# Kernel optimization log

Measured on AMD Instinct MI355X. Metric: run time of the kernel, lower is better.

The kernel has to match this reference:

```python
import jax, jax.numpy as jnp
import numpy as np

N = 100000      # nodes
E = 1600000     # edges
NF, EF = 8, 4   # raw node/edge feature dims
HID = 64        # hidden_dim
HEADS = 4
C = HID // HEADS  # per-head channels = 16
L = 3           # num_layers
NEG_SLOPE = 0.2 # PyG GATConv leaky_relu slope
LN_EPS = 1e-5


def setup_inputs():
    key = jax.random.key(0)
    ks = jax.random.split(key, 16)
    s = 0.1
    return {
        "x": jax.random.normal(ks[0], (N, NF), dtype=jnp.float32),
        "edge_index": jax.random.randint(ks[1], (2, E), 0, N, dtype=jnp.int32),
        "edge_attr": jax.random.normal(ks[2], (E, EF), dtype=jnp.float32),
        "node_w": jax.random.normal(ks[3], (NF, HID), dtype=jnp.float32) * s,
        "node_b": jnp.zeros((HID,), jnp.float32),
        "edge_w": jax.random.normal(ks[4], (EF, HID), dtype=jnp.float32) * s,
        "edge_b": jnp.zeros((HID,), jnp.float32),
        "lin_w": jax.random.normal(ks[5], (L, HID, HEADS * C), dtype=jnp.float32) * s,
        "lin_edge_w": jax.random.normal(ks[6], (L, HID, HEADS * C), dtype=jnp.float32) * s,
        "att_src": jax.random.normal(ks[7], (L, HEADS, C), dtype=jnp.float32) * s,
        "att_dst": jax.random.normal(ks[8], (L, HEADS, C), dtype=jnp.float32) * s,
        "att_edge": jax.random.normal(ks[9], (L, HEADS, C), dtype=jnp.float32) * s,
        "gat_bias": jnp.zeros((L, HID), jnp.float32),
        "ln_gamma": jnp.ones((L, HID), jnp.float32),
        "ln_beta": jnp.zeros((L, HID), jnp.float32),
    }


def _layer_norm(x, g, b):
    mu = jnp.mean(x, axis=-1, keepdims=True)
    var = jnp.mean(jnp.square(x - mu), axis=-1, keepdims=True)
    return (x - mu) * jax.lax.rsqrt(var + LN_EPS) * g + b


def _gat_conv(x, src, dst, e_proj, lin_w, lin_edge_w, a_src_w, a_dst_w, a_edge_w, bias):
    """PyG GATConv (concat=True, edge_dim, self-loops with fill='mean').
    x: [N,HID]; src/dst: [E'] (already include self loops); e_proj: [E',HID]."""
    n = x.shape[0]
    xs = (x @ lin_w).reshape(n, HEADS, C)                    # [N,H,C]
    ea = (e_proj @ lin_edge_w).reshape(-1, HEADS, C)         # [E',H,C]
    a_src = jnp.einsum('nhc,hc->nh', xs, a_src_w)            # [N,H]
    a_dst = jnp.einsum('nhc,hc->nh', xs, a_dst_w)            # [N,H]
    a_edge = jnp.einsum('ehc,hc->eh', ea, a_edge_w)          # [E',H]
    alpha = a_src[src] + a_dst[dst] + a_edge                 # [E',H]
    alpha = jax.nn.leaky_relu(alpha, NEG_SLOPE)
    # segment softmax over edges sharing a destination node
    amax = jax.ops.segment_max(alpha, dst, num_segments=n)   # [N,H]
    ex = jnp.exp(alpha - amax[dst])
    denom = jax.ops.segment_sum(ex, dst, num_segments=n)     # [N,H]
    w = ex / (denom[dst] + 1e-16)                            # [E',H]
    msg = xs[src] * w[:, :, None]                            # [E',H,C]
    out = jax.ops.segment_sum(msg, dst, num_segments=n)      # [N,H,C]
    return out.reshape(n, HEADS * C) + bias


def reference(x, edge_index, edge_attr, node_w, node_b, edge_w, edge_b,
              lin_w, lin_edge_w, att_src, att_dst, att_edge, gat_bias,
              ln_gamma, ln_beta):
    h = x @ node_w + node_b                                  # [N,HID]
    e = edge_attr @ edge_w + edge_b                          # [E,HID]
    src, dst = edge_index[0], edge_index[1]
    # add self loops once (same for all layers); edge_attr fill = per-dst mean
    ones = jnp.ones((E,), h.dtype)
    deg = jax.ops.segment_sum(ones, dst, num_segments=N)     # [N]
    e_mean = jax.ops.segment_sum(e, dst, num_segments=N) / jnp.maximum(deg, 1.0)[:, None]
    loop = jnp.arange(N, dtype=src.dtype)
    src_f = jnp.concatenate([src, loop])
    dst_f = jnp.concatenate([dst, loop])
    e_f = jnp.concatenate([e, e_mean], axis=0)               # [E+N,HID]
    for i in range(L):
        residual = h
        h = _gat_conv(h, src_f, dst_f, e_f, lin_w[i], lin_edge_w[i],
                      att_src[i], att_dst[i], att_edge[i], gat_bias[i])
        h = _layer_norm(h + residual, ln_gamma[i], ln_beta[i])
        h = jax.nn.relu(h)
    return h
```

## Files before the change

### kernel.cpp

```cpp
#include <hip/hip_runtime.h>


#define LRELU_SLOPE 0.2f
#define LOG2E 1.4426950408889634f
#define P1B 512
#define NBKT_MAX 512

typedef float f32x2 __attribute__((ext_vector_type(2)));

#ifdef __has_builtin
#if __has_builtin(__builtin_amdgcn_fdot2_f32_bf16)
#define HAS_BF16DOT 1
#endif
#endif
#ifndef HAS_BF16DOT
#define HAS_BF16DOT 0
#endif

#if HAS_BF16DOT
typedef __bf16 bf16x2_t __attribute__((ext_vector_type(2)));
#endif

__device__ __forceinline__ f32x2 fp8lo(unsigned int v) {
    return __builtin_amdgcn_cvt_pk_f32_fp8((int)v, false);
}
__device__ __forceinline__ f32x2 fp8hi(unsigned int v) {
    return __builtin_amdgcn_cvt_pk_f32_fp8((int)v, true);
}
__device__ __forceinline__ ushort f2bf(float x) {
    unsigned int b = __float_as_uint(x);
    return (ushort)((b + 0x7fffu + ((b >> 16) & 1u)) >> 16);
}
__device__ __forceinline__ unsigned int pack2bf(float a, float b) {
    return (unsigned int)f2bf(a) | ((unsigned int)f2bf(b) << 16);
}
__device__ __forceinline__ float bf_lo(unsigned int v) { return __uint_as_float(v << 16); }
__device__ __forceinline__ float bf_hi(unsigned int v) { return __uint_as_float(v & 0xffff0000u); }

__device__ __forceinline__ float dot2bf(unsigned int a, unsigned int b, float c) {
#if HAS_BF16DOT
    return __builtin_amdgcn_fdot2_f32_bf16(__builtin_bit_cast(bf16x2_t, a),
                                           __builtin_bit_cast(bf16x2_t, b), c, false);
#else
    return fmaf(bf_lo(a), bf_lo(b), fmaf(bf_hi(a), bf_hi(b), c));
#endif
}

__global__ void k_prep0(const float* __restrict__ lin_edge_w,
                        const float* __restrict__ att_edge,
                        const float* __restrict__ edge_w,
                        const float* __restrict__ edge_b,
                        float* __restrict__ Mc,
                        const float* __restrict__ x, const float* __restrict__ nw,
                        const float* __restrict__ nb, ushort* __restrict__ hbf,
                        int n_nodes)
{
    __shared__ float we[3][64][4];
    int t = threadIdx.x;
    if (blockIdx.x == 0) {
        if (t < 192) {
            int l = t >> 6, k = t & 63;
            for (int h = 0; h < 4; ++h) {
                float acc = 0.f;
                #pragma unroll
                for (int c = 0; c < 16; ++c)
                    acc = fmaf(lin_edge_w[l*4096 + k*64 + h*16 + c],
                               att_edge[l*64 + h*16 + c], acc);
                we[l][k][h] = acc;
            }
        }
        __syncthreads();
        if (t < 48) {
            int l = t >> 4, k4 = (t >> 2) & 3, h = t & 3;
            float acc = 0.f;
            for (int k = 0; k < 64; ++k)
                acc = fmaf(edge_w[k4*64 + k], we[l][k][h], acc);
            Mc[l*16 + k4*4 + h] = acc * LOG2E;
        }
        if (t >= 64 && t < 76) {
            int u = t - 64, l = u >> 2, h = u & 3;
            float acc = 0.f;
            for (int k = 0; k < 64; ++k)
                acc = fmaf(edge_b[k], we[l][k][h], acc);
            Mc[48 + l*4 + h] = acc * LOG2E;
        }
        return;
    }
    int idx = (blockIdx.x - 1) * blockDim.x + t;
    int n = idx >> 6, j = idx & 63;
    if (n >= n_nodes) return;
    float acc = nb[j];
    #pragma unroll
    for (int k = 0; k < 8; ++k) acc = fmaf(x[n*8 + k], nw[k*64 + j], acc);
    hbf[(size_t)n*64 + j] = f2bf(acc);
}

__global__ __launch_bounds__(256) void k_hist1(const int* __restrict__ dst,
                                               int* __restrict__ C,
                                               int E, int chunk, int nbkt) {
    __shared__ int h[NBKT_MAX];
    int b = blockIdx.x, t = threadIdx.x;
    for (int i = t; i < nbkt; i += 256) h[i] = 0;
    __syncthreads();
    int e0 = b*chunk, e1 = min(e0 + chunk, E);
    for (int e = e0 + t; e < e1; e += 256)
        atomicAdd(&h[dst[e] >> 8], 1);
    __syncthreads();
    for (int i = t; i < nbkt; i += 256) C[i*P1B + b] = h[i];
}

__global__ void k_scanA(const int* __restrict__ in, int* __restrict__ out,
                        int* __restrict__ bsum, int n) {
    __shared__ int s[1024];
    int i = blockIdx.x*1024 + threadIdx.x;
    s[threadIdx.x] = (i < n) ? in[i] : 0;
    __syncthreads();
    for (int off = 1; off < 1024; off <<= 1) {
        int t = (threadIdx.x >= off) ? s[threadIdx.x - off] : 0;
        __syncthreads();
        s[threadIdx.x] += t;
        __syncthreads();
    }
    if (i < n) out[i] = s[threadIdx.x];
    if (threadIdx.x == 1023) bsum[blockIdx.x] = s[1023];
}

__global__ void k_scanB(int* bsum, int nb) {
    __shared__ int s[1024];
    int t = threadIdx.x;
    int own = (t < nb) ? bsum[t] : 0;
    s[t] = own;
    __syncthreads();
    for (int off = 1; off < 1024; off <<= 1) {
        int v = (t >= off) ? s[t - off] : 0;
        __syncthreads();
        s[t] += v;
        __syncthreads();
    }
    if (t < nb) bsum[t] = s[t] - own;
}

__device__ __forceinline__ int scanned(const int* S, const int* bsum, int idx) {
    return S[idx] + bsum[idx >> 10];
}

__global__ __launch_bounds__(256) void k_scat1(const int* __restrict__ dst,
        const int* __restrict__ srcv, const float4* __restrict__ ea,
        const int* __restrict__ S, const int* __restrict__ bsum,
        uint2* __restrict__ brec, int E, int chunk, int nbkt) {
    __shared__ int base[NBKT_MAX];
    __shared__ int cur[NBKT_MAX];
    int b = blockIdx.x, t = threadIdx.x;
    for (int i = t; i < nbkt; i += 256) {
        int flat = i*P1B + b;
        base[i] = flat ? scanned(S, bsum, flat - 1) : 0;
        cur[i] = 0;
    }
    __syncthreads();
    int e0 = b*chunk, e1 = min(e0 + chunk, E);
    for (int e = e0 + t; e < e1; e += 256) {
        int d = dst[e];
        int bin = d >> 8;
        int lr = atomicAdd(&cur[bin], 1);
        int slot = base[bin] + lr;
        float4 v = ea[e];
        unsigned int p = (unsigned int)__builtin_amdgcn_cvt_pk_fp8_f32(v.x, v.y, 0, false);
        p = (unsigned int)__builtin_amdgcn_cvt_pk_fp8_f32(v.z, v.w, (int)p, true);
        uint2 r;
        r.x = (unsigned int)srcv[e] | ((unsigned int)(d & 255) << 24);
        r.y = p;
        brec[slot] = r;
    }
}

__global__ __launch_bounds__(256) void k_csr(const uint2* __restrict__ brec,
        const int* __restrict__ S, const int* __restrict__ bsum,
        uint2* __restrict__ recs, int* __restrict__ rowptr, int* __restrict__ perm,
        float4* __restrict__ ea_mean, int nbkt, int NN, int E) {
    int bkt = blockIdx.x, t = threadIdx.x;
    __shared__ int cnt[256], exc[256], cur[256], ssc[256], dk[256];
    int ib = bkt*P1B - 1, ie = (bkt + 1)*P1B - 1;
    int seg_b = bkt ? scanned(S, bsum, ib) : 0;
    int seg_e = scanned(S, bsum, ie);
    cnt[t] = 0; cur[t] = 0;
    __syncthreads();
    for (int i = seg_b + t; i < seg_e; i += 256)
        atomicAdd(&cnt[brec[i].x >> 24], 1);
    __syncthreads();
    ssc[t] = cnt[t];
    __syncthreads();
    for (int off = 1; off < 256; off <<= 1) {
        int v = (t >= off) ? ssc[t - off] : 0;
        __syncthreads();
        ssc[t] += v;
        __syncthreads();
    }
    exc[t] = ssc[t] - cnt[t];
    __syncthreads();
    int g = bkt*256 + t;
    bool valid = (g < NN);
    int row_b = seg_b + exc[t];
    if (valid) rowptr[g] = row_b;
    if (bkt == nbkt - 1 && t == 0) rowptr[NN] = E;
    int myd = valid ? cnt[t] : 0x7FFFFFFF;
    dk[t] = myd;
    __syncthreads();
    int w0 = t & ~15;
    int rank = 0;
    #pragma unroll
    for (int j = 0; j < 16; ++j) {
        int od = dk[w0 + j];
        rank += (int)((od < myd) || (od == myd && (w0 + j) < t));
    }
    perm[bkt*256 + w0 + rank] = g;
    for (int i = seg_b + t; i < seg_e; i += 256) {
        uint2 r = brec[i];
        int dl = (int)(r.x >> 24);
        int slot = seg_b + exc[dl] + atomicAdd(&cur[dl], 1);
        r.x &= 0x00FFFFFFu;
        recs[slot] = r;
    }
    __syncthreads();
    if (valid) {
        int deg = cnt[t];
        float sx = 0.f, sy = 0.f, sz = 0.f, sw = 0.f;
        for (int i = 0; i < deg; ++i) {
            unsigned int p = recs[row_b + i].y;
            f32x2 lo = fp8lo(p), hi = fp8hi(p);
            sx += lo.x; sy += lo.y; sz += hi.x; sw += hi.y;
        }
        float inv = deg ? 1.f / (float)deg : 0.f;
        ea_mean[g] = make_float4(sx*inv, sy*inv, sz*inv, sw*inv);
    }
    if (bkt == nbkt - 1 && t < 8 && E > 0) recs[E + t] = recs[E - 1];
}

__global__ __launch_bounds__(256) void k_proj(const ushort* __restrict__ hbf,
        const float* __restrict__ lw,
        const float* __restrict__ asw,
        const float* __restrict__ adw,
        ushort* __restrict__ xs2, float* __restrict__ a_src4,
        float* __restrict__ a_dst4, int n_nodes)
{
    __shared__ unsigned int Wp[2048];
    for (int i = threadIdx.x; i < 2048; i += 256) {
        int k2 = i >> 6, c = i & 63;
        Wp[i] = pack2bf(lw[(k2*2)*64 + c], lw[(k2*2+1)*64 + c]);
    }
    __syncthreads();
    int lane = threadIdx.x & 63, wid = threadIdx.x >> 6;
    float as_w = asw[lane] * LOG2E, ad_w = adw[lane] * LOG2E;
    int nquads = (n_nodes + 3) >> 2;
    int nlast = n_nodes - 1;
    for (int q = blockIdx.x*4 + wid; q < nquads; q += gridDim.x*4) {
        int n0 = q << 2;
        int n1 = min(n0+1, nlast), n2 = min(n0+2, nlast), n3 = min(n0+3, nlast);
        const uint4* r0p = (const uint4*)(hbf + (size_t)n0*64);
        const uint4* r1p = (const uint4*)(hbf + (size_t)n1*64);
        const uint4* r2p = (const uint4*)(hbf + (size_t)n2*64);
        const uint4* r3p = (const uint4*)(hbf + (size_t)n3*64);
        float acc0 = 0.f, acc1 = 0.f, acc2 = 0.f, acc3 = 0.f;
        #pragma unroll
        for (int qq = 0; qq < 8; ++qq) {
            uint4 u0 = r0p[qq], u1 = r1p[qq], u2 = r2p[qq], u3 = r3p[qq];
            unsigned int w0 = Wp[(qq*4+0)*64 + lane];
            unsigned int w1 = Wp[(qq*4+1)*64 + lane];
            unsigned int w2 = Wp[(qq*4+2)*64 + lane];
            unsigned int w3 = Wp[(qq*4+3)*64 + lane];
            acc0 = dot2bf(u0.w, w3, dot2bf(u0.z, w2, dot2bf(u0.y, w1, dot2bf(u0.x, w0, acc0))));
            acc1 = dot2bf(u1.w, w3, dot2bf(u1.z, w2, dot2bf(u1.y, w1, dot2bf(u1.x, w0, acc1))));
            acc2 = dot2bf(u2.w, w3, dot2bf(u2.z, w2, dot2bf(u2.y, w1, dot2bf(u2.x, w0, acc2))));
            acc3 = dot2bf(u3.w, w3, dot2bf(u3.z, w2, dot2bf(u3.y, w1, dot2bf(u3.x, w0, acc3))));
        }
        xs2[(size_t)n0*64 + lane] = f2bf(acc0);
        xs2[(size_t)n1*64 + lane] = f2bf(acc1);
        xs2[(size_t)n2*64 + lane] = f2bf(acc2);
        xs2[(size_t)n3*64 + lane] = f2bf(acc3);
        #define ARED(ACC, NJ) { \
            float ps = (ACC)*as_w, pd = (ACC)*ad_w; \
            ps += __shfl_xor(ps,1,16); pd += __shfl_xor(pd,1,16); \
            ps += __shfl_xor(ps,2,16); pd += __shfl_xor(pd,2,16); \
            ps += __shfl_xor(ps,4,16); pd += __shfl_xor(pd,4,16); \
            ps += __shfl_xor(ps,8,16); pd += __shfl_xor(pd,8,16); \
            if ((lane & 15) == 0) { \
                a_src4[(NJ)*4 + (lane>>4)] = ps; \
                a_dst4[(NJ)*4 + (lane>>4)] = pd; \
            } }
        ARED(acc0, n0) ARED(acc1, n1) ARED(acc2, n2) ARED(acc3, n3)
        #undef ARED
    }
}

__global__ __launch_bounds__(256) void k_gat(const uint4* __restrict__ xs4,
        const float* __restrict__ a_src4, const float* __restrict__ a_dst4,
        const int* __restrict__ rowptr, const uint2* __restrict__ recs,
        const float4* __restrict__ ea_mean, const int* __restrict__ perm,
        const float* __restrict__ Mc,
        const float* __restrict__ c0,
        const float* __restrict__ bias, const float* __restrict__ lng,
        const float* __restrict__ lnb,
        const ushort* __restrict__ hbf_in, ushort* __restrict__ hbf_out,
        float* __restrict__ out_f32, int last, int n_nodes)
{
    int lane = threadIdx.x & 63;
    int q4 = lane >> 4;
    int gq = blockIdx.x*16 + (threadIdx.x >> 6)*4 + q4;
    bool active = (gq < n_nodes);
    int n = active ? perm[gq] : 0;
    int l4  = lane & 15;
    int k8  = l4 & 7;
    int hB  = k8 >> 1;
    int grp = l4 >> 3;
    int cb = k8 * 8;
    uint4 rr = *(const uint4*)(hbf_in + (size_t)n*64 + cb);
    float4 eam = ea_mean[n];
    float m0 = Mc[hB], m1 = Mc[4+hB], m2 = Mc[8+hB], m3 = Mc[12+hB];
    float c0v = c0[hB];
    float adv = a_dst4[n*4 + hB];
    float cc = c0v + adv;
    int rb = rowptr[n], re = active ? rowptr[n + 1] : rb;

    float denL = 0.f;
    float a0=0.f,a1=0.f,a2=0.f,a3=0.f,a4=0.f,a5=0.f,a6=0.f,a7=0.f;

    if (rb < re) {
        int bmax = re - grp;
        uint2 rc = recs[rb + grp];
        uint2 rn = recs[rb + 2 + grp];
        float asc = a_src4[(int)rc.x*4 + hB];
        uint4 xc = xs4[(unsigned)rc.x*8u + (unsigned)k8];
        #pragma unroll 2
        for (int b = rb; b < re; b += 2) {
            uint2 r2 = recs[b + 4 + grp];
            float asn = a_src4[(int)rn.x*4 + hB];
            uint4 xn = xs4[(unsigned)rn.x*8u + (unsigned)k8];
            f32x2 e01 = fp8lo(rc.y), e23 = fp8hi(rc.y);
            float al = fmaf(e01.x, m0, fmaf(e01.y, m1,
                       fmaf(e23.x, m2, fmaf(e23.y, m3, cc)))) + asc;
            al = fmaxf(al, LRELU_SLOPE * al);
            float ev = (b < bmax) ? exp2f(al) : 0.f;
            denL += ev;
            a0 = fmaf(bf_lo(xc.x), ev, a0); a1 = fmaf(bf_hi(xc.x), ev, a1);
            a2 = fmaf(bf_lo(xc.y), ev, a2); a3 = fmaf(bf_hi(xc.y), ev, a3);
            a4 = fmaf(bf_lo(xc.z), ev, a4); a5 = fmaf(bf_hi(xc.z), ev, a5);
            a6 = fmaf(bf_lo(xc.w), ev, a6); a7 = fmaf(bf_hi(xc.w), ev, a7);
            rc = rn; rn = r2; asc = asn; xc = xn;
        }
    }
    denL += __shfl_xor(denL, 8);
    a0 += __shfl_xor(a0, 8); a1 += __shfl_xor(a1, 8);
    a2 += __shfl_xor(a2, 8); a3 += __shfl_xor(a3, 8);
    a4 += __shfl_xor(a4, 8); a5 += __shfl_xor(a5, 8);
    a6 += __shfl_xor(a6, 8); a7 += __shfl_xor(a7, 8);
    float ael = (re > rb)
        ? fmaf(eam.x, m0, fmaf(eam.y, m1, fmaf(eam.z, m2, fmaf(eam.w, m3, c0v))))
        : 0.f;
    float alS = a_src4[n*4 + hB] + adv + ael;
    alS = fmaxf(alS, LRELU_SLOPE * alS);
    float evS = exp2f(alS);
    float denF = denL + evS;
    uint4 vs = xs4[(unsigned)n*8u + (unsigned)k8];
    a0 = fmaf(bf_lo(vs.x), evS, a0); a1 = fmaf(bf_hi(vs.x), evS, a1);
    a2 = fmaf(bf_lo(vs.y), evS, a2); a3 = fmaf(bf_hi(vs.y), evS, a3);
    a4 = fmaf(bf_lo(vs.z), evS, a4); a5 = fmaf(bf_hi(vs.z), evS, a5);
    a6 = fmaf(bf_lo(vs.w), evS, a6); a7 = fmaf(bf_hi(vs.w), evS, a7);
    float inv = 1.f / (denF + 1e-16f);
    const float4* bp = (const float4*)(bias + cb);
    float4 b0 = bp[0], b1 = bp[1];
    float o0 = a0*inv + b0.x + bf_lo(rr.x), o1 = a1*inv + b0.y + bf_hi(rr.x);
    float o2 = a2*inv + b0.z + bf_lo(rr.y), o3 = a3*inv + b0.w + bf_hi(rr.y);
    float o4 = a4*inv + b1.x + bf_lo(rr.z), o5 = a5*inv + b1.y + bf_hi(rr.z);
    float o6 = a6*inv + b1.z + bf_lo(rr.w), o7 = a7*inv + b1.w + bf_hi(rr.w);
    float s1 = o0+o1+o2+o3+o4+o5+o6+o7;
    s1 += __shfl_xor(s1, 1); s1 += __shfl_xor(s1, 2); s1 += __shfl_xor(s1, 4);
    float mu = s1 * 0.015625f;
    float d0=o0-mu,d1=o1-mu,d2=o2-mu,d3=o3-mu,d4=o4-mu,d5=o5-mu,d6=o6-mu,d7=o7-mu;
    float s2 = d0*d0+d1*d1+d2*d2+d3*d3+d4*d4+d5*d5+d6*d6+d7*d7;
    s2 += __shfl_xor(s2, 1); s2 += __shfl_xor(s2, 2); s2 += __shfl_xor(s2, 4);
    float rs = rsqrtf(s2 * 0.015625f + 1e-5f);
    const float4* gp = (const float4*)(lng + cb);
    const float4* zp = (const float4*)(lnb + cb);
    float4 g0 = gp[0], g1 = gp[1], z0 = zp[0], z1 = zp[1];
    float y0 = fmaxf(d0*rs*g0.x + z0.x, 0.f), y1 = fmaxf(d1*rs*g0.y + z0.y, 0.f);
    float y2 = fmaxf(d2*rs*g0.z + z0.z, 0.f), y3 = fmaxf(d3*rs*g0.w + z0.w, 0.f);
    float y4 = fmaxf(d4*rs*g1.x + z1.x, 0.f), y5 = fmaxf(d5*rs*g1.y + z1.y, 0.f);
    float y6 = fmaxf(d6*rs*g1.z + z1.z, 0.f), y7 = fmaxf(d7*rs*g1.w + z1.w, 0.f);
    if (grp == 0 && active) {
        if (last) {
            float4* outp = (float4*)(out_f32 + (size_t)n*64 + cb);
            outp[0] = make_float4(y0, y1, y2, y3);
            outp[1] = make_float4(y4, y5, y6, y7);
        } else {
            uint4 pk;
            pk.x = pack2bf(y0, y1); pk.y = pack2bf(y2, y3);
            pk.z = pack2bf(y4, y5); pk.w = pack2bf(y6, y7);
            *(uint4*)(hbf_out + (size_t)n*64 + cb) = pk;
        }
    }
}

extern "C" void kernel_launch(void* const* d_in, const int* in_sizes, int n_in,
                              void* d_out, int out_size, void* d_ws, size_t ws_size,
                              hipStream_t stream) {
    const float* x          = (const float*)d_in[0];
    const int*   ei         = (const int*)d_in[1];
    const float* edge_attr  = (const float*)d_in[2];
    const float* node_w     = (const float*)d_in[3];
    const float* node_b     = (const float*)d_in[4];
    const float* edge_w     = (const float*)d_in[5];
    const float* edge_b     = (const float*)d_in[6];
    const float* lin_w      = (const float*)d_in[7];
    const float* lin_edge_w = (const float*)d_in[8];
    const float* att_src    = (const float*)d_in[9];
    const float* att_dst    = (const float*)d_in[10];
    const float* att_edge   = (const float*)d_in[11];
    const float* gat_bias   = (const float*)d_in[12];
    const float* ln_g       = (const float*)d_in[13];
    const float* ln_b       = (const float*)d_in[14];

    int NN = in_sizes[0] / 8;
    int E  = in_sizes[1] / 2;
    const int* src = ei;
    const int* dst = ei + E;

    int nbkt = (NN + 255) >> 8;
    int ntot = nbkt * P1B;
    int chunk = (E + P1B - 1) / P1B;

    char* wsp = (char*)d_ws;
    size_t off = 0;
    auto alloc = [&](size_t bytes) -> void* {
        off = (off + 255) & ~(size_t)255;
        void* p = wsp + off;
        off += bytes;
        return p;
    };
    ushort* h_bf    = (ushort*)alloc((size_t)NN * 64 * 2);
    ushort* xs2     = (ushort*)alloc((size_t)NN * 64 * 2);
    float*  a_src4  = (float*)alloc((size_t)NN * 4 * 4);
    float*  a_dst4  = (float*)alloc((size_t)NN * 4 * 4);
    uint2*  recs    = (uint2*)alloc((size_t)(E + 8) * 8);
    uint2*  brec    = (uint2*)alloc((size_t)E * 8);
    float4* ea_mean = (float4*)alloc((size_t)NN * 16);
    int*    rowptr  = (int*)alloc((size_t)(NN + 1) * 4);
    int*    perm    = (int*)alloc((size_t)(nbkt * 256) * 4);
    int*    S       = (int*)alloc((size_t)ntot * 4);
    int*    bsum    = (int*)alloc(4096);
    float*  Mc      = (float*)alloc(256);

    k_prep0<<<1 + (NN*64 + 255) / 256, 256, 0, stream>>>(
        lin_edge_w, att_edge, edge_w, edge_b, Mc, x, node_w, node_b, h_bf, NN);
    k_hist1<<<P1B, 256, 0, stream>>>(dst, S, E, chunk, nbkt);
    int nsb = (ntot + 1023) / 1024;
    k_scanA<<<nsb, 1024, 0, stream>>>(S, S, bsum, ntot);
    k_scanB<<<1, 1024, 0, stream>>>(bsum, nsb);
    k_scat1<<<P1B, 256, 0, stream>>>(dst, src, (const float4*)edge_attr,
                                     S, bsum, brec, E, chunk, nbkt);
    k_csr<<<nbkt, 256, 0, stream>>>(brec, S, bsum, recs, rowptr, perm, ea_mean,
                                    nbkt, NN, E);

    for (int l = 0; l < 3; ++l) {
        k_proj<<<2048, 256, 0, stream>>>(h_bf, lin_w + l*4096, att_src + l*64,
                                         att_dst + l*64, xs2, a_src4, a_dst4, NN);
        k_gat<<<(NN + 15) / 16, 256, 0, stream>>>((const uint4*)xs2, a_src4, a_dst4,
                                                  rowptr, recs, ea_mean, perm,
                                                  Mc + l*16, Mc + 48 + l*4,
                                                  gat_bias + l*64, ln_g + l*64, ln_b + l*64,
                                                  h_bf, h_bf, (float*)d_out,
                                                  (l == 2) ? 1 : 0, NN);
    }
}
```

Before: 317.7 us.

## Merge histogram into prep, fuse layer-0 projection with CSR build, deepen gather prefetch

Folds the dst histogram kernel into the prep kernel and runs the first layer's node projection in extra blocks of the CSR-build kernel, so independent work shares launches and can overlap. The GAT aggregation loop now prefetches one more edge record, source attention value and feature row. The goal is fewer kernel launches and more memory latency hidden in the gather loop, at the cost of extra registers and larger shared memory per block in the merged kernels, which may lower occupancy.

```diff
diff --git a/kernel.cpp b/kernel.cpp
--- a/kernel.cpp
+++ b/kernel.cpp
@@ -5,6 +5,7 @@
 #define LOG2E 1.4426950408889634f
 #define P1B 512
 #define NBKT_MAX 512
+#define PROJB 2048
 
 typedef float f32x2 __attribute__((ext_vector_type(2)));
 
@@ -46,213 +47,22 @@
 #endif
 }
 
-__global__ void k_prep0(const float* __restrict__ lin_edge_w,
-                        const float* __restrict__ att_edge,
-                        const float* __restrict__ edge_w,
-                        const float* __restrict__ edge_b,
-                        float* __restrict__ Mc,
-                        const float* __restrict__ x, const float* __restrict__ nw,
-                        const float* __restrict__ nb, ushort* __restrict__ hbf,
-                        int n_nodes)
+__device__ __forceinline__ void proj_body(int pb, int t,
+        const ushort* __restrict__ hbf, const float* __restrict__ lw,
+        const float* __restrict__ asw, const float* __restrict__ adw,
+        ushort* __restrict__ xs2, float* __restrict__ a_src4,
+        float* __restrict__ a_dst4, int n_nodes, unsigned int* Wp)
 {
-    __shared__ float we[3][64][4];
-    int t = threadIdx.x;
-    if (blockIdx.x == 0) {
-        if (t < 192) {
-            int l = t >> 6, k = t & 63;
-            for (int h = 0; h < 4; ++h) {
-                float acc = 0.f;
-                #pragma unroll
-                for (int c = 0; c < 16; ++c)
-                    acc = fmaf(lin_edge_w[l*4096 + k*64 + h*16 + c],
-                               att_edge[l*64 + h*16 + c], acc);
-                we[l][k][h] = acc;
-            }
-        }
-        __syncthreads();
-        if (t < 48) {
-            int l = t >> 4, k4 = (t >> 2) & 3, h = t & 3;
-            float acc = 0.f;
-            for (int k = 0; k < 64; ++k)
-                acc = fmaf(edge_w[k4*64 + k], we[l][k][h], acc);
-            Mc[l*16 + k4*4 + h] = acc * LOG2E;
-        }
-        if (t >= 64 && t < 76) {
-            int u = t - 64, l = u >> 2, h = u & 3;
-            float acc = 0.f;
-            for (int k = 0; k < 64; ++k)
-                acc = fmaf(edge_b[k], we[l][k][h], acc);
-            Mc[48 + l*4 + h] = acc * LOG2E;
-        }
-        return;
-    }
-    int idx = (blockIdx.x - 1) * blockDim.x + t;
-    int n = idx >> 6, j = idx & 63;
-    if (n >= n_nodes) return;
-    float acc = nb[j];
-    #pragma unroll
-    for (int k = 0; k < 8; ++k) acc = fmaf(x[n*8 + k], nw[k*64 + j], acc);
-    hbf[(size_t)n*64 + j] = f2bf(acc);
-}
-
-__global__ __launch_bounds__(256) void k_hist1(const int* __restrict__ dst,
-                                               int* __restrict__ C,
-                                               int E, int chunk, int nbkt) {
-    __shared__ int h[NBKT_MAX];
-    int b = blockIdx.x, t = threadIdx.x;
-    for (int i = t; i < nbkt; i += 256) h[i] = 0;
-    __syncthreads();
-    int e0 = b*chunk, e1 = min(e0 + chunk, E);
-    for (int e = e0 + t; e < e1; e += 256)
-        atomicAdd(&h[dst[e] >> 8], 1);
-    __syncthreads();
-    for (int i = t; i < nbkt; i += 256) C[i*P1B + b] = h[i];
-}
-
-__global__ void k_scanA(const int* __restrict__ in, int* __restrict__ out,
-                        int* __restrict__ bsum, int n) {
-    __shared__ int s[1024];
-    int i = blockIdx.x*1024 + threadIdx.x;
-    s[threadIdx.x] = (i < n) ? in[i] : 0;
-    __syncthreads();
-    for (int off = 1; off < 1024; off <<= 1) {
-        int t = (threadIdx.x >= off) ? s[threadIdx.x - off] : 0;
-        __syncthreads();
-        s[threadIdx.x] += t;
-        __syncthreads();
-    }
-    if (i < n) out[i] = s[threadIdx.x];
-    if (threadIdx.x == 1023) bsum[blockIdx.x] = s[1023];
-}
-
-__global__ void k_scanB(int* bsum, int nb) {
-    __shared__ int s[1024];
-    int t = threadIdx.x;
-    int own = (t < nb) ? bsum[t] : 0;
-    s[t] = own;
-    __syncthreads();
-    for (int off = 1; off < 1024; off <<= 1) {
-        int v = (t >= off) ? s[t - off] : 0;
-        __syncthreads();
-        s[t] += v;
-        __syncthreads();
-    }
-    if (t < nb) bsum[t] = s[t] - own;
-}
-
-__device__ __forceinline__ int scanned(const int* S, const int* bsum, int idx) {
-    return S[idx] + bsum[idx >> 10];
-}
-
-__global__ __launch_bounds__(256) void k_scat1(const int* __restrict__ dst,
-        const int* __restrict__ srcv, const float4* __restrict__ ea,
-        const int* __restrict__ S, const int* __restrict__ bsum,
-        uint2* __restrict__ brec, int E, int chunk, int nbkt) {
-    __shared__ int base[NBKT_MAX];
-    __shared__ int cur[NBKT_MAX];
-    int b = blockIdx.x, t = threadIdx.x;
-    for (int i = t; i < nbkt; i += 256) {
-        int flat = i*P1B + b;
-        base[i] = flat ? scanned(S, bsum, flat - 1) : 0;
-        cur[i] = 0;
-    }
-    __syncthreads();
-    int e0 = b*chunk, e1 = min(e0 + chunk, E);
-    for (int e = e0 + t; e < e1; e += 256) {
-        int d = dst[e];
-        int bin = d >> 8;
-        int lr = atomicAdd(&cur[bin], 1);
-        int slot = base[bin] + lr;
-        float4 v = ea[e];
-        unsigned int p = (unsigned int)__builtin_amdgcn_cvt_pk_fp8_f32(v.x, v.y, 0, false);
-        p = (unsigned int)__builtin_amdgcn_cvt_pk_fp8_f32(v.z, v.w, (int)p, true);
-        uint2 r;
-        r.x = (unsigned int)srcv[e] | ((unsigned int)(d & 255) << 24);
-        r.y = p;
-        brec[slot] = r;
-    }
-}
-
-__global__ __launch_bounds__(256) void k_csr(const uint2* __restrict__ brec,
-        const int* __restrict__ S, const int* __restrict__ bsum,
-        uint2* __restrict__ recs, int* __restrict__ rowptr, int* __restrict__ perm,
-        float4* __restrict__ ea_mean, int nbkt, int NN, int E) {
-    int bkt = blockIdx.x, t = threadIdx.x;
-    __shared__ int cnt[256], exc[256], cur[256], ssc[256], dk[256];
-    int ib = bkt*P1B - 1, ie = (bkt + 1)*P1B - 1;
-    int seg_b = bkt ? scanned(S, bsum, ib) : 0;
-    int seg_e = scanned(S, bsum, ie);
-    cnt[t] = 0; cur[t] = 0;
-    __syncthreads();
-    for (int i = seg_b + t; i < seg_e; i += 256)
-        atomicAdd(&cnt[brec[i].x >> 24], 1);
-    __syncthreads();
-    ssc[t] = cnt[t];
-    __syncthreads();
-    for (int off = 1; off < 256; off <<= 1) {
-        int v = (t >= off) ? ssc[t - off] : 0;
-        __syncthreads();
-        ssc[t] += v;
-        __syncthreads();
-    }
-    exc[t] = ssc[t] - cnt[t];
-    __syncthreads();
-    int g = bkt*256 + t;
-    bool valid = (g < NN);
-    int row_b = seg_b + exc[t];
-    if (valid) rowptr[g] = row_b;
-    if (bkt == nbkt - 1 && t == 0) rowptr[NN] = E;
-    int myd = valid ? cnt[t] : 0x7FFFFFFF;
-    dk[t] = myd;
-    __syncthreads();
-    int w0 = t & ~15;
-    int rank = 0;
-    #pragma unroll
-    for (int j = 0; j < 16; ++j) {
-        int od = dk[w0 + j];
-        rank += (int)((od < myd) || (od == myd && (w0 + j) < t));
-    }
-    perm[bkt*256 + w0 + rank] = g;
-    for (int i = seg_b + t; i < seg_e; i += 256) {
-        uint2 r = brec[i];
-        int dl = (int)(r.x >> 24);
-        int slot = seg_b + exc[dl] + atomicAdd(&cur[dl], 1);
-        r.x &= 0x00FFFFFFu;
-        recs[slot] = r;
-    }
-    __syncthreads();
-    if (valid) {
-        int deg = cnt[t];
-        float sx = 0.f, sy = 0.f, sz = 0.f, sw = 0.f;
-        for (int i = 0; i < deg; ++i) {
-            unsigned int p = recs[row_b + i].y;
-            f32x2 lo = fp8lo(p), hi = fp8hi(p);
-            sx += lo.x; sy += lo.y; sz += hi.x; sw += hi.y;
-        }
-        float inv = deg ? 1.f / (float)deg : 0.f;
-        ea_mean[g] = make_float4(sx*inv, sy*inv, sz*inv, sw*inv);
-    }
-    if (bkt == nbkt - 1 && t < 8 && E > 0) recs[E + t] = recs[E - 1];
-}
-
-__global__ __launch_bounds__(256) void k_proj(const ushort* __restrict__ hbf,
-        const float* __restrict__ lw,
-        const float* __restrict__ asw,
-        const float* __restrict__ adw,
-        ushort* __restrict__ xs2, float* __restrict__ a_src4,
-        float* __restrict__ a_dst4, int n_nodes)
-{
-    __shared__ unsigned int Wp[2048];
-    for (int i = threadIdx.x; i < 2048; i += 256) {
+    for (int i = t; i < 2048; i += 256) {
         int k2 = i >> 6, c = i & 63;
         Wp[i] = pack2bf(lw[(k2*2)*64 + c], lw[(k2*2+1)*64 + c]);
     }
     __syncthreads();
-    int lane = threadIdx.x & 63, wid = threadIdx.x >> 6;
+    int lane = t & 63, wid = t >> 6;
     float as_w = asw[lane] * LOG2E, ad_w = adw[lane] * LOG2E;
     int nquads = (n_nodes + 3) >> 2;
     int nlast = n_nodes - 1;
-    for (int q = blockIdx.x*4 + wid; q < nquads; q += gridDim.x*4) {
+    for (int q = pb*4 + wid; q < nquads; q += PROJB*4) {
         int n0 = q << 2;
         int n1 = min(n0+1, nlast), n2 = min(n0+2, nlast), n3 = min(n0+3, nlast);
         const uint4* r0p = (const uint4*)(hbf + (size_t)n0*64);
@@ -289,6 +99,216 @@
         ARED(acc0, n0) ARED(acc1, n1) ARED(acc2, n2) ARED(acc3, n3)
         #undef ARED
     }
+}
+
+__global__ __launch_bounds__(256) void k_prep0(const float* __restrict__ lin_edge_w,
+                        const float* __restrict__ att_edge,
+                        const float* __restrict__ edge_w,
+                        const float* __restrict__ edge_b,
+                        float* __restrict__ Mc,
+                        const float* __restrict__ x, const float* __restrict__ nw,
+                        const float* __restrict__ nb, ushort* __restrict__ hbf,
+                        const int* __restrict__ dst, int* __restrict__ C,
+                        int E, int chunk, int nbkt, int n_nodes)
+{
+    __shared__ float we[3][64][4];
+    __shared__ int hh[NBKT_MAX];
+    int t = threadIdx.x;
+    if (blockIdx.x == 0) {
+        if (t < 192) {
+            int l = t >> 6, k = t & 63;
+            for (int h = 0; h < 4; ++h) {
+                float acc = 0.f;
+                #pragma unroll
+                for (int c = 0; c < 16; ++c)
+                    acc = fmaf(lin_edge_w[l*4096 + k*64 + h*16 + c],
+                               att_edge[l*64 + h*16 + c], acc);
+                we[l][k][h] = acc;
+            }
+        }
+        __syncthreads();
+        if (t < 48) {
+            int l = t >> 4, k4 = (t >> 2) & 3, h = t & 3;
+            float acc = 0.f;
+            for (int k = 0; k < 64; ++k)
+                acc = fmaf(edge_w[k4*64 + k], we[l][k][h], acc);
+            Mc[l*16 + k4*4 + h] = acc * LOG2E;
+        }
+        if (t >= 64 && t < 76) {
+            int u = t - 64, l = u >> 2, h = u & 3;
+            float acc = 0.f;
+            for (int k = 0; k < 64; ++k)
+                acc = fmaf(edge_b[k], we[l][k][h], acc);
+            Mc[48 + l*4 + h] = acc * LOG2E;
+        }
+        return;
+    }
+    if (blockIdx.x <= P1B) {
+        int b = blockIdx.x - 1;
+        for (int i = t; i < nbkt; i += 256) hh[i] = 0;
+        __syncthreads();
+        int e0 = b*chunk, e1 = min(e0 + chunk, E);
+        for (int e = e0 + t; e < e1; e += 256)
+            atomicAdd(&hh[dst[e] >> 8], 1);
+        __syncthreads();
+        for (int i = t; i < nbkt; i += 256) C[i*P1B + b] = hh[i];
+        return;
+    }
+    int idx = (blockIdx.x - 1 - P1B) * 256 + t;
+    int n = idx >> 6, j = idx & 63;
+    if (n >= n_nodes) return;
+    float acc = nb[j];
+    #pragma unroll
+    for (int k = 0; k < 8; ++k) acc = fmaf(x[n*8 + k], nw[k*64 + j], acc);
+    hbf[(size_t)n*64 + j] = f2bf(acc);
+}
+
+__global__ void k_scanA(const int* __restrict__ in, int* __restrict__ out,
+                        int* __restrict__ bsum, int n) {
+    __shared__ int s[1024];
+    int i = blockIdx.x*1024 + threadIdx.x;
+    s[threadIdx.x] = (i < n) ? in[i] : 0;
+    __syncthreads();
+    for (int off = 1; off < 1024; off <<= 1) {
+        int t = (threadIdx.x >= off) ? s[threadIdx.x - off] : 0;
+        __syncthreads();
+        s[threadIdx.x] += t;
+        __syncthreads();
+    }
+    if (i < n) out[i] = s[threadIdx.x];
+    if (threadIdx.x == 1023) bsum[blockIdx.x] = s[1023];
+}
+
+__global__ void k_scanB(int* bsum, int nb) {
+    __shared__ int s[1024];
+    int t = threadIdx.x;
+    int own = (t < nb) ? bsum[t] : 0;
+    s[t] = own;
+    __syncthreads();
+    for (int off = 1; off < 1024; off <<= 1) {
+        int v = (t >= off) ? s[t - off] : 0;
+        __syncthreads();
+        s[t] += v;
+        __syncthreads();
+    }
+    if (t < nb) bsum[t] = s[t] - own;
+}
+
+__device__ __forceinline__ int scanned(const int* S, const int* bsum, int idx) {
+    return S[idx] + bsum[idx >> 10];
+}
+
+__global__ __launch_bounds__(256) void k_scat1(const int* __restrict__ dst,
+        const int* __restrict__ srcv, const float4* __restrict__ ea,
+        const int* __restrict__ S, const int* __restrict__ bsum,
+        uint2* __restrict__ brec, int E, int chunk, int nbkt) {
+    __shared__ int base[NBKT_MAX];
+    __shared__ int cur[NBKT_MAX];
+    int b = blockIdx.x, t = threadIdx.x;
+    for (int i = t; i < nbkt; i += 256) {
+        int flat = i*P1B + b;
+        base[i] = flat ? scanned(S, bsum, flat - 1) : 0;
+        cur[i] = 0;
+    }
+    __syncthreads();
+    int e0 = b*chunk, e1 = min(e0 + chunk, E);
+    for (int e = e0 + t; e < e1; e += 256) {
+        int d = dst[e];
+        int bin = d >> 8;
+        int lr = atomicAdd(&cur[bin], 1);
+        int slot = base[bin] + lr;
+        float4 v = ea[e];
+        unsigned int p = (unsigned int)__builtin_amdgcn_cvt_pk_fp8_f32(v.x, v.y, 0, false);
+        p = (unsigned int)__builtin_amdgcn_cvt_pk_fp8_f32(v.z, v.w, (int)p, true);
+        uint2 r;
+        r.x = (unsigned int)srcv[e] | ((unsigned int)(d & 255) << 24);
+        r.y = p;
+        brec[slot] = r;
+    }
+}
+
+__global__ __launch_bounds__(256) void k_csrproj(const uint2* __restrict__ brec,
+        const int* __restrict__ S, const int* __restrict__ bsum,
+        uint2* __restrict__ recs, int* __restrict__ rowptr, int* __restrict__ perm,
+        float4* __restrict__ ea_mean, int nbkt, int NN, int E,
+        const ushort* __restrict__ hbf, const float* __restrict__ lw,
+        const float* __restrict__ asw, const float* __restrict__ adw,
+        ushort* __restrict__ xs2, float* __restrict__ a_src4,
+        float* __restrict__ a_dst4)
+{
+    __shared__ int cnt[256], exc[256], cur[256], ssc[256], dk[256];
+    __shared__ unsigned int Wp[2048];
+    int t = threadIdx.x;
+    if (blockIdx.x >= nbkt) {
+        proj_body(blockIdx.x - nbkt, t, hbf, lw, asw, adw,
+                  xs2, a_src4, a_dst4, NN, Wp);
+        return;
+    }
+    int bkt = blockIdx.x;
+    int ib = bkt*P1B - 1, ie = (bkt + 1)*P1B - 1;
+    int seg_b = bkt ? scanned(S, bsum, ib) : 0;
+    int seg_e = scanned(S, bsum, ie);
+    cnt[t] = 0; cur[t] = 0;
+    __syncthreads();
+    for (int i = seg_b + t; i < seg_e; i += 256)
+        atomicAdd(&cnt[brec[i].x >> 24], 1);
+    __syncthreads();
+    ssc[t] = cnt[t];
+    __syncthreads();
+    for (int off = 1; off < 256; off <<= 1) {
+        int v = (t >= off) ? ssc[t - off] : 0;
+        __syncthreads();
+        ssc[t] += v;
+        __syncthreads();
+    }
+    exc[t] = ssc[t] - cnt[t];
+    __syncthreads();
+    int g = bkt*256 + t;
+    bool valid = (g < NN);
+    int row_b = seg_b + exc[t];
+    if (valid) rowptr[g] = row_b;
+    if (bkt == nbkt - 1 && t == 0) rowptr[NN] = E;
+    int myd = valid ? cnt[t] : 0x7FFFFFFF;
+    dk[t] = myd;
+    __syncthreads();
+    int w0 = t & ~15;
+    int rank = 0;
+    #pragma unroll
+    for (int j = 0; j < 16; ++j) {
+        int od = dk[w0 + j];
+        rank += (int)((od < myd) || (od == myd && (w0 + j) < t));
+    }
+    perm[bkt*256 + w0 + rank] = g;
+    for (int i = seg_b + t; i < seg_e; i += 256) {
+        uint2 r = brec[i];
+        int dl = (int)(r.x >> 24);
+        int slot = seg_b + exc[dl] + atomicAdd(&cur[dl], 1);
+        r.x &= 0x00FFFFFFu;
+        recs[slot] = r;
+    }
+    __syncthreads();
+    if (valid) {
+        int deg = cnt[t];
+        float sx = 0.f, sy = 0.f, sz = 0.f, sw = 0.f;
+        for (int i = 0; i < deg; ++i) {
+            unsigned int p = recs[row_b + i].y;
+            f32x2 lo = fp8lo(p), hi = fp8hi(p);
+            sx += lo.x; sy += lo.y; sz += hi.x; sw += hi.y;
+        }
+        float inv = deg ? 1.f / (float)deg : 0.f;
+        ea_mean[g] = make_float4(sx*inv, sy*inv, sz*inv, sw*inv);
+    }
+    if (bkt == nbkt - 1 && t < 8 && E > 0) recs[E + t] = recs[E - 1];
+}
+
+__global__ __launch_bounds__(256) void k_proj(const ushort* __restrict__ hbf,
+        const float* __restrict__ lw, const float* __restrict__ asw,
+        const float* __restrict__ adw, ushort* __restrict__ xs2,
+        float* __restrict__ a_src4, float* __restrict__ a_dst4, int n_nodes)
+{
+    __shared__ unsigned int Wp[2048];
+    proj_body(blockIdx.x, threadIdx.x, hbf, lw, asw, adw,
+              xs2, a_src4, a_dst4, n_nodes, Wp);
 }
 
 __global__ __launch_bounds__(256) void k_gat(const uint4* __restrict__ xs4,
@@ -327,13 +347,16 @@
         int bmax = re - grp;
         uint2 rc = recs[rb + grp];
         uint2 rn = recs[rb + 2 + grp];
+        uint2 r2 = recs[rb + 4 + grp];
         float asc = a_src4[(int)rc.x*4 + hB];
+        float asn = a_src4[(int)rn.x*4 + hB];
         uint4 xc = xs4[(unsigned)rc.x*8u + (unsigned)k8];
+        uint4 xn = xs4[(unsigned)rn.x*8u + (unsigned)k8];
         #pragma unroll 2
         for (int b = rb; b < re; b += 2) {
-            uint2 r2 = recs[b + 4 + grp];
-            float asn = a_src4[(int)rn.x*4 + hB];
-            uint4 xn = xs4[(unsigned)rn.x*8u + (unsigned)k8];
+            uint2 r3 = recs[b + 6 + grp];
+            float as2 = a_src4[(int)r2.x*4 + hB];
+            uint4 x2 = xs4[(unsigned)r2.x*8u + (unsigned)k8];
             f32x2 e01 = fp8lo(rc.y), e23 = fp8hi(rc.y);
             float al = fmaf(e01.x, m0, fmaf(e01.y, m1,
                        fmaf(e23.x, m2, fmaf(e23.y, m3, cc)))) + asc;
@@ -344,7 +367,9 @@
             a2 = fmaf(bf_lo(xc.y), ev, a2); a3 = fmaf(bf_hi(xc.y), ev, a3);
             a4 = fmaf(bf_lo(xc.z), ev, a4); a5 = fmaf(bf_hi(xc.z), ev, a5);
             a6 = fmaf(bf_lo(xc.w), ev, a6); a7 = fmaf(bf_hi(xc.w), ev, a7);
-            rc = rn; rn = r2; asc = asn; xc = xn;
+            rc = rn; rn = r2; r2 = r3;
+            asc = asn; asn = as2;
+            xc = xn; xn = x2;
         }
     }
     denL += __shfl_xor(denL, 8);
@@ -448,20 +473,24 @@
     int*    bsum    = (int*)alloc(4096);
     float*  Mc      = (float*)alloc(256);
 
-    k_prep0<<<1 + (NN*64 + 255) / 256, 256, 0, stream>>>(
-        lin_edge_w, att_edge, edge_w, edge_b, Mc, x, node_w, node_b, h_bf, NN);
-    k_hist1<<<P1B, 256, 0, stream>>>(dst, S, E, chunk, nbkt);
+    int nodeb = (NN*64 + 255) / 256;
+    k_prep0<<<1 + P1B + nodeb, 256, 0, stream>>>(
+        lin_edge_w, att_edge, edge_w, edge_b, Mc, x, node_w, node_b, h_bf,
+        dst, S, E, chunk, nbkt, NN);
     int nsb = (ntot + 1023) / 1024;
     k_scanA<<<nsb, 1024, 0, stream>>>(S, S, bsum, ntot);
     k_scanB<<<1, 1024, 0, stream>>>(bsum, nsb);
     k_scat1<<<P1B, 256, 0, stream>>>(dst, src, (const float4*)edge_attr,
                                      S, bsum, brec, E, chunk, nbkt);
-    k_csr<<<nbkt, 256, 0, stream>>>(brec, S, bsum, recs, rowptr, perm, ea_mean,
-                                    nbkt, NN, E);
+    k_csrproj<<<nbkt + PROJB, 256, 0, stream>>>(brec, S, bsum, recs, rowptr, perm,
+                                                ea_mean, nbkt, NN, E,
+                                                h_bf, lin_w, att_src, att_dst,
+                                                xs2, a_src4, a_dst4);
 
     for (int l = 0; l < 3; ++l) {
-        k_proj<<<2048, 256, 0, stream>>>(h_bf, lin_w + l*4096, att_src + l*64,
-                                         att_dst + l*64, xs2, a_src4, a_dst4, NN);
+        if (l > 0)
+            k_proj<<<PROJB, 256, 0, stream>>>(h_bf, lin_w + l*4096, att_src + l*64,
+                                              att_dst + l*64, xs2, a_src4, a_dst4, NN);
         k_gat<<<(NN + 15) / 16, 256, 0, stream>>>((const uint4*)xs2, a_src4, a_dst4,
                                                   rowptr, recs, ea_mean, perm,
                                                   Mc + l*16, Mc + 48 + l*4,
```

Result: faster. 303.6 us, median of 2 (-4.4%).
